# Kernel tuning notes

Measured on AMD Instinct MI355X. Metric: run time of the kernel, lower is better.

Reference implementation:

```python
import jax, jax.numpy as jnp
import numpy as np

B, S, E, H, HD, RD, MP = 2, 2048, 1024, 16, 64, 32, 8  # batch, seq, embed, heads, head_dim, rotary_dim, mp_num


def rotate_every_two(x):
    # x: [..., D] -> interleave (-x_odd, x_even)
    x1 = x[..., ::2]
    x2 = x[..., 1::2]
    return jnp.stack((-x2, x1), axis=-1).reshape(x.shape)


def apply_rotary(x, sin, cos):
    # x: [B,S,H,RD]; sin/cos: [S, RD//2] -> repeat_interleave(2) -> [1,S,1,RD]
    sin = jnp.repeat(sin, 2, axis=-1)[None, :, None, :]
    cos = jnp.repeat(cos, 2, axis=-1)[None, :, None, :]
    return x * cos + rotate_every_two(x) * sin


def setup_inputs() -> dict:
    key = jax.random.key(0)
    k1, k2, k3 = jax.random.split(key, 3)
    return {
        "hidden_states": jax.random.normal(k1, (B, S, E), dtype=jnp.float32),
        "w_qkv": jax.random.normal(k2, (3 * E, E), dtype=jnp.float32) * 0.02,
        "w_out": jax.random.normal(k3, (E, E), dtype=jnp.float32) * 0.02,
    }


def reference(hidden_states, w_qkv, w_out):
    qkv = hidden_states @ w_qkv.T                      # [B,S,3E]
    local = HD * H // MP                               # 128
    qkv = qkv.reshape(B, S, MP, 3 * local)
    # torch.split order in source is (query, value, key)
    q, v, k = jnp.split(qkv, 3, axis=-1)               # each [B,S,MP,local]

    def split_heads(x):
        return x.reshape(B, S, MP, H // MP, HD).reshape(B, S, H, HD)

    q, k, v = split_heads(q), split_heads(k), split_heads(v)  # [B,S,H,HD]

    # fixed sinusoidal rotary embedding over first RD dims
    inv_freq = 1.0 / 10000 ** (jnp.arange(0, RD, 2, dtype=jnp.float32) / RD)
    sinusoid = jnp.arange(S, dtype=jnp.float32)[:, None] * inv_freq[None, :]  # [S, RD//2]
    sin, cos = jnp.sin(sinusoid), jnp.cos(sinusoid)

    q = jnp.concatenate([apply_rotary(q[..., :RD], sin, cos), q[..., RD:]], axis=-1)
    k = jnp.concatenate([apply_rotary(k[..., :RD], sin, cos), k[..., RD:]], axis=-1)

    # [B,H,S,HD]
    q = q.transpose(0, 2, 1, 3)
    k = k.transpose(0, 2, 1, 3)
    v = v.transpose(0, 2, 1, 3)

    scores = jnp.einsum('bhqd,bhkd->bhqk', q, k) / np.float32(np.sqrt(HD))
    causal = jnp.tril(jnp.ones((S, S), dtype=bool))
    scores = jnp.where(causal[None, None], scores, jnp.float32(-1e9))
    attn = jax.nn.softmax(scores.astype(jnp.float32), axis=-1).astype(q.dtype)
    out = jnp.einsum('bhqk,bhkd->bhqd', attn, v)       # [B,H,S,HD]
    out = out.transpose(0, 2, 1, 3).reshape(B, S, E)
    return out @ w_out.T
```

## Files before the change

### kernel.cpp

```cpp
#include <hip/hip_runtime.h>

typedef __attribute__((ext_vector_type(8))) short short8;
typedef __attribute__((ext_vector_type(4))) float v4f;

#define ASYNC_COPY16(ldsptr, gptr)                                                        \
  __builtin_amdgcn_global_load_lds((const __attribute__((address_space(1))) void*)(gptr), \
                                   (__attribute__((address_space(3))) void*)(ldsptr),     \
                                   16, 0, 0)

__device__ __forceinline__ unsigned short f2bf(float f) {
  unsigned int u = __float_as_uint(f);
  u += 0x7fffu + ((u >> 16) & 1u);
  return (unsigned short)(u >> 16);
}
__device__ __forceinline__ float bf2f(unsigned short s) {
  return __uint_as_float(((unsigned int)s) << 16);
}

__global__ void convert_all(const float* __restrict__ h, const float* __restrict__ wq,
                            const float* __restrict__ wo, unsigned short* __restrict__ ho,
                            unsigned short* __restrict__ wqo, unsigned short* __restrict__ woo) {
  int i = (blockIdx.x * blockDim.x + threadIdx.x) * 4;
  const float* src;
  unsigned short* dst;
  int j;
  if (i < 4194304) { src = h; dst = ho; j = i; }
  else if (i < 7340032) { src = wq; dst = wqo; j = i - 4194304; }
  else { src = wo; dst = woo; j = i - 7340032; }
  float4 v = *(const float4*)(src + j);
  ushort4 o;
  o.x = f2bf(v.x); o.y = f2bf(v.y); o.z = f2bf(v.z); o.w = f2bf(v.w);
  *(ushort4*)(dst + j) = o;
}

template <int BN, bool BF16OUT>
__global__ __launch_bounds__(256) void gemm_bt(const unsigned short* __restrict__ A,
                                               const unsigned short* __restrict__ Bm,
                                               void* __restrict__ Cv, int M, int N, int K) {
  constexpr int WN = BN / 2;
  constexpr int JN = WN / 16;
  __shared__ __attribute__((aligned(16))) unsigned short As[128 * 32];
  __shared__ __attribute__((aligned(16))) unsigned short Bs[BN * 32];
  int t = threadIdx.x;
  int w = t >> 6, lane = t & 63, kb = lane >> 4, lr = lane & 15;
  int m0 = blockIdx.y * 128, n0 = blockIdx.x * BN;
  int wm = (w >> 1) * 64, wn = (w & 1) * WN;
  v4f acc[4][JN];
#pragma unroll
  for (int i = 0; i < 4; i++)
#pragma unroll
    for (int j = 0; j < JN; j++) acc[i][j] = (v4f){0.f, 0.f, 0.f, 0.f};
  int ra = m0 + (t >> 2);
  int rb = n0 + (t >> 2);
  int ca = (t & 3) * 8;
  for (int k0 = 0; k0 < K; k0 += 32) {
    ASYNC_COPY16(&As[t * 8],        A + (size_t)ra * K + k0 + ca);
    ASYNC_COPY16(&As[2048 + t * 8], A + (size_t)(ra + 64) * K + k0 + ca);
#pragma unroll
    for (int c = 0; c < BN / 64; c++)
      ASYNC_COPY16(&Bs[c * 2048 + t * 8], Bm + (size_t)(rb + c * 64) * K + k0 + ca);
    __syncthreads();
    short8 av[4], bv[JN];
#pragma unroll
    for (int i = 0; i < 4; i++) av[i] = *(const short8*)&As[(wm + i * 16 + lr) * 32 + kb * 8];
#pragma unroll
    for (int j = 0; j < JN; j++) bv[j] = *(const short8*)&Bs[(wn + j * 16 + lr) * 32 + kb * 8];
#pragma unroll
    for (int i = 0; i < 4; i++)
#pragma unroll
      for (int j = 0; j < JN; j++)
        acc[i][j] = __builtin_amdgcn_mfma_f32_16x16x32_bf16(av[i], bv[j], acc[i][j], 0, 0, 0);
    __syncthreads();
  }
#pragma unroll
  for (int i = 0; i < 4; i++) {
    int row = m0 + wm + i * 16 + kb * 4;
#pragma unroll
    for (int j = 0; j < JN; j++) {
      int col = n0 + wn + j * 16 + lr;
#pragma unroll
      for (int r = 0; r < 4; r++) {
        if (BF16OUT)
          ((unsigned short*)Cv)[(size_t)(row + r) * N + col] = f2bf(acc[i][j][r]);
        else
          ((float*)Cv)[(size_t)(row + r) * N + col] = acc[i][j][r];
      }
    }
  }
}

__global__ __launch_bounds__(256) void rope_vt(const unsigned short* __restrict__ qkv,
                                               unsigned short* __restrict__ Q,
                                               unsigned short* __restrict__ Ko,
                                               unsigned short* __restrict__ Vt) {
  __shared__ float tile[64][65];
  int t = threadIdx.x;
  int bh = blockIdx.y, s0 = blockIdx.x * 64;
  int b = bh >> 4, h = bh & 15;
  int mp = h >> 1, ii = h & 1;
  int hbase = mp * 384 + ii * 64;
  int tx = t & 63, ty = t >> 6;
#pragma unroll
  for (int q16 = 0; q16 < 16; q16++) {
    int srow = q16 * 4 + ty;
    tile[srow][tx] = bf2f(qkv[(size_t)(b * 2048 + s0 + srow) * 3072 + hbase + 128 + tx]);
  }
  int sl = t >> 2, ch = t & 3;
  int s = s0 + sl;
  size_t ib = (size_t)(b * 2048 + s) * 3072 + hbase + ch * 16;
  short8 qv0 = *(const short8*)(qkv + ib);
  short8 qv1 = *(const short8*)(qkv + ib + 8);
  short8 kv0 = *(const short8*)(qkv + ib + 256);
  short8 kv1 = *(const short8*)(qkv + ib + 264);
  float qf[16], kf[16];
#pragma unroll
  for (int j = 0; j < 8; j++) {
    qf[j] = bf2f((unsigned short)qv0[j]); qf[8 + j] = bf2f((unsigned short)qv1[j]);
    kf[j] = bf2f((unsigned short)kv0[j]); kf[8 + j] = bf2f((unsigned short)kv1[j]);
  }
  if (ch < 2) {
#pragma unroll
    for (int jj = 0; jj < 8; jj++) {
      int j = ch * 8 + jj;
      float ang = (float)s * expf(-(float)j * 0.57564627324851142f);
      float sn, cs;
      sincosf(ang, &sn, &cs);
      float a = qf[2 * jj], bq = qf[2 * jj + 1];
      qf[2 * jj] = a * cs - bq * sn; qf[2 * jj + 1] = bq * cs + a * sn;
      float c2 = kf[2 * jj], d2 = kf[2 * jj + 1];
      kf[2 * jj] = c2 * cs - d2 * sn; kf[2 * jj + 1] = d2 * cs + c2 * sn;
    }
  }
  const float qs = 0.125f * 1.4426950408889634f;
  unsigned short qo[16], ko[16];
#pragma unroll
  for (int j = 0; j < 16; j++) { qo[j] = f2bf(qs * qf[j]); ko[j] = f2bf(kf[j]); }
  size_t ob = (size_t)(bh * 2048 + s) * 64 + ch * 16;
  *(short8*)(Q + ob) = *(short8*)qo;
  *(short8*)(Q + ob + 8) = *(short8*)(qo + 8);
  *(short8*)(Ko + ob) = *(short8*)ko;
  *(short8*)(Ko + ob + 8) = *(short8*)(ko + 8);
  __syncthreads();
#pragma unroll
  for (int q16 = 0; q16 < 16; q16++) {
    int drow = q16 * 4 + ty;
    Vt[(size_t)bh * 64 * 2048 + (size_t)drow * 2048 + s0 + tx] = f2bf(tile[tx][drow]);
  }
}

__global__ __launch_bounds__(256) void attn_fused(const unsigned short* __restrict__ Qg,
                                                  const unsigned short* __restrict__ Kg,
                                                  const unsigned short* __restrict__ Vtg,
                                                  unsigned short* __restrict__ AO) {
  __shared__ __attribute__((aligned(16))) unsigned short Ks[2 * 128 * 64];
  __shared__ __attribute__((aligned(16))) unsigned short Vs[2 * 64 * 128];
  __shared__ __attribute__((aligned(16))) unsigned short Ps[4 * 32 * 64];
  int t = threadIdx.x;
  int w = t >> 6, lane = t & 63, kb = lane >> 4, lr = lane & 15;
  int wq = w >> 1, wk = w & 1;
  int gid = blockIdx.x;
  int bh = gid >> 4, pr = gid & 15;
  const unsigned short* Qb = Qg + (size_t)bh * 2048 * 64;
  const unsigned short* Kb = Kg + (size_t)bh * 2048 * 64;
  const unsigned short* Vb = Vtg + (size_t)bh * 64 * 2048;
  int b = bh >> 4, h = bh & 15;
  int sw = lr & 7;
  unsigned short* Pw = &Ps[w * 32 * 64];
  float* accS = (float*)Ps;
  float* lpS = (float*)Ks;

  auto stage = [&](int kt, int buf) {
    int base = buf * 8192;
#pragma unroll
    for (int rep = 0; rep < 4; rep++) {
      int s = rep * 256 + t;
      int krow = s >> 3;
      int kgc = (s & 7) ^ (krow & 7);
      ASYNC_COPY16(&Ks[base + s * 8], Kb + (size_t)(kt * 128 + krow) * 64 + kgc * 8);
      int vrow = s >> 4;
      int vgc = (s & 15) ^ (vrow & 7);
      ASYNC_COPY16(&Vs[base + s * 8], Vb + (size_t)vrow * 2048 + kt * 128 + vgc * 8);
    }
  };

  for (int half = 0; half < 2; half++) {
    int qtile = half ? (31 - pr) : pr;
    int m0 = qtile * 64;
    int nkt = (qtile >> 1) + 1;
    short8 aq[2][2];
#pragma unroll
    for (int m = 0; m < 2; m++) {
      int row = m0 + wq * 32 + m * 16 + lr;
#pragma unroll
      for (int c = 0; c < 2; c++)
        aq[m][c] = *(const short8*)(Qb + (size_t)row * 64 + c * 32 + kb * 8);
    }
    v4f acc[2][4];
    v4f lp[2];
#pragma unroll
    for (int m = 0; m < 2; m++) {
      lp[m] = (v4f){0.f, 0.f, 0.f, 0.f};
#pragma unroll
      for (int dt = 0; dt < 4; dt++) acc[m][dt] = (v4f){0.f, 0.f, 0.f, 0.f};
    }
    stage(0, 0);
    __syncthreads();
    for (int kt = 0; kt < nkt; kt++) {
      int cur = (kt & 1) * 8192;
      if (kt + 1 < nkt) stage(kt + 1, (kt + 1) & 1);
      v4f sc[2][4];
#pragma unroll
      for (int n = 0; n < 4; n++) {
        int krow = wk * 64 + n * 16 + lr;
        short8 bk0 = *(const short8*)&Ks[cur + krow * 64 + ((kb) ^ sw) * 8];
        short8 bk1 = *(const short8*)&Ks[cur + krow * 64 + ((kb + 4) ^ sw) * 8];
#pragma unroll
        for (int m = 0; m < 2; m++) {
          v4f z = (v4f){0.f, 0.f, 0.f, 0.f};
          z = __builtin_amdgcn_mfma_f32_16x16x32_bf16(aq[m][0], bk0, z, 0, 0, 0);
          z = __builtin_amdgcn_mfma_f32_16x16x32_bf16(aq[m][1], bk1, z, 0, 0, 0);
          sc[m][n] = z;
        }
      }
      if (kt == nkt - 1) {
#pragma unroll
        for (int m = 0; m < 2; m++)
#pragma unroll
          for (int n = 0; n < 4; n++)
#pragma unroll
            for (int r = 0; r < 4; r++) {
              int keya = kt * 128 + wk * 64 + n * 16 + lr;
              int qrow = m0 + wq * 32 + m * 16 + kb * 4 + r;
              if (keya > qrow) sc[m][n][r] = -1e30f;
            }
      }
#pragma unroll
      for (int m = 0; m < 2; m++)
#pragma unroll
        for (int n = 0; n < 4; n++)
#pragma unroll
          for (int r = 0; r < 4; r++) {
            float p = exp2f(sc[m][n][r]);
            lp[m][r] += p;
            int rp = m * 16 + kb * 4 + r;
            Pw[rp * 64 + ((n * 2 + (lr >> 3)) ^ (rp & 7)) * 8 + (lr & 7)] = f2bf(p);
          }
#pragma unroll
      for (int ks = 0; ks < 2; ks++) {
        short8 ap[2];
#pragma unroll
        for (int m = 0; m < 2; m++)
          ap[m] = *(const short8*)&Pw[(m * 16 + lr) * 64 + ((ks * 4 + kb) ^ sw) * 8];
#pragma unroll
        for (int dt = 0; dt < 4; dt++) {
          int d = dt * 16 + lr;
          short8 bv = *(const short8*)&Vs[cur + d * 128 + ((wk * 8 + ks * 4 + kb) ^ sw) * 8];
#pragma unroll
          for (int m = 0; m < 2; m++)
            acc[m][dt] = __builtin_amdgcn_mfma_f32_16x16x32_bf16(ap[m], bv, acc[m][dt], 0, 0, 0);
        }
      }
      __syncthreads();
    }
    if (wk == 1) {
#pragma unroll
      for (int m = 0; m < 2; m++) {
#pragma unroll
        for (int dt = 0; dt < 4; dt++)
          *(v4f*)&accS[wq * 2048 + (m * 4 + dt) * 256 + lane * 4] = acc[m][dt];
        *(v4f*)&lpS[wq * 512 + lane * 8 + m * 4] = lp[m];
      }
    }
    __syncthreads();
    if (wk == 0) {
#pragma unroll
      for (int m = 0; m < 2; m++) {
#pragma unroll
        for (int dt = 0; dt < 4; dt++)
          acc[m][dt] += *(v4f*)&accS[wq * 2048 + (m * 4 + dt) * 256 + lane * 4];
        lp[m] += *(v4f*)&lpS[wq * 512 + lane * 8 + m * 4];
      }
#pragma unroll
      for (int m = 0; m < 2; m++)
#pragma unroll
        for (int r = 0; r < 4; r++) {
          float s = lp[m][r];
#pragma unroll
          for (int off = 1; off < 16; off <<= 1) s += __shfl_xor(s, off);
          float inv = 1.0f / s;
          int qrow = m0 + wq * 32 + m * 16 + kb * 4 + r;
#pragma unroll
          for (int dt = 0; dt < 4; dt++)
            AO[(size_t)(b * 2048 + qrow) * 1024 + h * 64 + dt * 16 + lr] =
                f2bf(acc[m][dt][r] * inv);
        }
    }
    __syncthreads();
  }
}

extern "C" void kernel_launch(void* const* d_in, const int* in_sizes, int n_in,
                              void* d_out, int out_size, void* d_ws, size_t ws_size,
                              hipStream_t stream) {
  const float* hidden = (const float*)d_in[0];
  const float* w_qkv = (const float*)d_in[1];
  const float* w_out = (const float*)d_in[2];
  float* out = (float*)d_out;
  char* ws = (char*)d_ws;
  unsigned short* hid_bf = (unsigned short*)(ws);
  unsigned short* wqkv_bf = (unsigned short*)(ws + (8ull << 20));
  unsigned short* wout_bf = (unsigned short*)(ws + (14ull << 20));
  unsigned short* qkv_bf = (unsigned short*)(ws + (16ull << 20));
  unsigned short* Qb = (unsigned short*)(ws + (40ull << 20));
  unsigned short* Kb = (unsigned short*)(ws + (48ull << 20));
  unsigned short* Vt = (unsigned short*)(ws + (56ull << 20));
  unsigned short* AO = (unsigned short*)(ws + (64ull << 20));

  convert_all<<<8192, 256, 0, stream>>>(hidden, w_qkv, w_out, hid_bf, wqkv_bf, wout_bf);
  gemm_bt<128, true><<<dim3(24, 32), 256, 0, stream>>>(hid_bf, wqkv_bf, qkv_bf, 4096, 3072, 1024);
  rope_vt<<<dim3(32, 32), 256, 0, stream>>>(qkv_bf, Qb, Kb, Vt);
  attn_fused<<<512, 256, 0, stream>>>(Qb, Kb, Vt, AO);
  gemm_bt<64, false><<<dim3(16, 32), 256, 0, stream>>>(AO, wout_bf, out, 4096, 1024, 1024);
}
```

Before: 226.9 us.

## Restructure attention into one query tile per 128-thread block with 64-key tiles

The attention kernel no longer has each 256-thread block process a paired short and long query tile, with two wave pairs splitting the keys and merging partial results through LDS. It now launches 1024 blocks of 128 threads, each handling one 64-row query tile over 64-key tiles, with a rotated tile order to spread causal work. The per-block cross-wave reduction is gone. V is written in a permuted column order so each lane can store four packed bf16 P values at once, turning scalar LDS stores into 8-byte stores. The cost is less intra-block parallelism, more blocks with uneven causal work, and more loop iterations per key.

```diff
diff --git a/kernel.cpp b/kernel.cpp
--- a/kernel.cpp
+++ b/kernel.cpp
@@ -144,159 +144,142 @@
 #pragma unroll
   for (int q16 = 0; q16 < 16; q16++) {
     int drow = q16 * 4 + ty;
-    Vt[(size_t)bh * 64 * 2048 + (size_t)drow * 2048 + s0 + tx] = f2bf(tile[tx][drow]);
-  }
-}
-
-__global__ __launch_bounds__(256) void attn_fused(const unsigned short* __restrict__ Qg,
+    int p = (tx & 15) * 4 + (tx >> 4);
+    Vt[(size_t)bh * 64 * 2048 + (size_t)drow * 2048 + s0 + p] = f2bf(tile[tx][drow]);
+  }
+}
+
+__global__ __launch_bounds__(128) void attn_fused(const unsigned short* __restrict__ Qg,
                                                   const unsigned short* __restrict__ Kg,
                                                   const unsigned short* __restrict__ Vtg,
                                                   unsigned short* __restrict__ AO) {
-  __shared__ __attribute__((aligned(16))) unsigned short Ks[2 * 128 * 64];
-  __shared__ __attribute__((aligned(16))) unsigned short Vs[2 * 64 * 128];
-  __shared__ __attribute__((aligned(16))) unsigned short Ps[4 * 32 * 64];
+  __shared__ __attribute__((aligned(16))) unsigned short Ks[2 * 64 * 64];
+  __shared__ __attribute__((aligned(16))) unsigned short Vs[2 * 64 * 64];
+  __shared__ __attribute__((aligned(16))) unsigned short Ps[2 * 32 * 64];
   int t = threadIdx.x;
   int w = t >> 6, lane = t & 63, kb = lane >> 4, lr = lane & 15;
-  int wq = w >> 1, wk = w & 1;
   int gid = blockIdx.x;
-  int bh = gid >> 4, pr = gid & 15;
+  int bh = gid >> 5;
+  int qtile = ((gid & 31) + bh) & 31;
+  int m0 = qtile * 64;
   const unsigned short* Qb = Qg + (size_t)bh * 2048 * 64;
   const unsigned short* Kb = Kg + (size_t)bh * 2048 * 64;
   const unsigned short* Vb = Vtg + (size_t)bh * 64 * 2048;
-  int b = bh >> 4, h = bh & 15;
+
+  short8 aq[2][2];
+#pragma unroll
+  for (int m = 0; m < 2; m++) {
+    int row = m0 + w * 32 + m * 16 + lr;
+#pragma unroll
+    for (int c = 0; c < 2; c++)
+      aq[m][c] = *(const short8*)(Qb + (size_t)row * 64 + c * 32 + kb * 8);
+  }
+
+  v4f acc[2][4];
+  float lp[2][4];
+#pragma unroll
+  for (int m = 0; m < 2; m++) {
+#pragma unroll
+    for (int dt = 0; dt < 4; dt++) acc[m][dt] = (v4f){0.f, 0.f, 0.f, 0.f};
+#pragma unroll
+    for (int r = 0; r < 4; r++) lp[m][r] = 0.f;
+  }
+
+  int nkt = qtile + 1;
+
+  auto stage = [&](int kt, int buf) {
+    int base = buf * 4096;
+#pragma unroll
+    for (int rep = 0; rep < 4; rep++) {
+      int s = rep * 128 + t;
+      int row = s >> 3;
+      int gc = (s & 7) ^ (row & 7);
+      ASYNC_COPY16(&Ks[base + s * 8], Kb + (size_t)(kt * 64 + row) * 64 + gc * 8);
+      ASYNC_COPY16(&Vs[base + s * 8], Vb + (size_t)row * 2048 + kt * 64 + gc * 8);
+    }
+  };
+
+  stage(0, 0);
+  __syncthreads();
+
   int sw = lr & 7;
   unsigned short* Pw = &Ps[w * 32 * 64];
-  float* accS = (float*)Ps;
-  float* lpS = (float*)Ks;
-
-  auto stage = [&](int kt, int buf) {
-    int base = buf * 8192;
-#pragma unroll
-    for (int rep = 0; rep < 4; rep++) {
-      int s = rep * 256 + t;
-      int krow = s >> 3;
-      int kgc = (s & 7) ^ (krow & 7);
-      ASYNC_COPY16(&Ks[base + s * 8], Kb + (size_t)(kt * 128 + krow) * 64 + kgc * 8);
-      int vrow = s >> 4;
-      int vgc = (s & 15) ^ (vrow & 7);
-      ASYNC_COPY16(&Vs[base + s * 8], Vb + (size_t)vrow * 2048 + kt * 128 + vgc * 8);
-    }
-  };
-
-  for (int half = 0; half < 2; half++) {
-    int qtile = half ? (31 - pr) : pr;
-    int m0 = qtile * 64;
-    int nkt = (qtile >> 1) + 1;
-    short8 aq[2][2];
-#pragma unroll
-    for (int m = 0; m < 2; m++) {
-      int row = m0 + wq * 32 + m * 16 + lr;
-#pragma unroll
-      for (int c = 0; c < 2; c++)
-        aq[m][c] = *(const short8*)(Qb + (size_t)row * 64 + c * 32 + kb * 8);
-    }
-    v4f acc[2][4];
-    v4f lp[2];
-#pragma unroll
-    for (int m = 0; m < 2; m++) {
-      lp[m] = (v4f){0.f, 0.f, 0.f, 0.f};
-#pragma unroll
-      for (int dt = 0; dt < 4; dt++) acc[m][dt] = (v4f){0.f, 0.f, 0.f, 0.f};
-    }
-    stage(0, 0);
+  for (int kt = 0; kt < nkt; kt++) {
+    int cur = (kt & 1) * 4096;
+    if (kt + 1 < nkt) stage(kt + 1, (kt + 1) & 1);
+    v4f sc[2][4];
+#pragma unroll
+    for (int n2 = 0; n2 < 4; n2++) {
+      int krow = n2 * 16 + lr;
+      short8 bk0 = *(const short8*)&Ks[cur + krow * 64 + (kb ^ sw) * 8];
+      short8 bk1 = *(const short8*)&Ks[cur + krow * 64 + ((kb + 4) ^ sw) * 8];
+#pragma unroll
+      for (int m = 0; m < 2; m++) {
+        v4f z = (v4f){0.f, 0.f, 0.f, 0.f};
+        z = __builtin_amdgcn_mfma_f32_16x16x32_bf16(aq[m][0], bk0, z, 0, 0, 0);
+        z = __builtin_amdgcn_mfma_f32_16x16x32_bf16(aq[m][1], bk1, z, 0, 0, 0);
+        sc[m][n2] = z;
+      }
+    }
+    if (kt == nkt - 1) {
+#pragma unroll
+      for (int m = 0; m < 2; m++)
+#pragma unroll
+        for (int n2 = 0; n2 < 4; n2++)
+#pragma unroll
+          for (int r = 0; r < 4; r++) {
+            int key = kt * 64 + n2 * 16 + lr;
+            int qrow = m0 + w * 32 + m * 16 + kb * 4 + r;
+            if (key > qrow) sc[m][n2][r] = -1e30f;
+          }
+    }
+#pragma unroll
+    for (int m = 0; m < 2; m++)
+#pragma unroll
+      for (int r = 0; r < 4; r++) {
+        unsigned short pk[4];
+#pragma unroll
+        for (int n2 = 0; n2 < 4; n2++) {
+          float p = exp2f(sc[m][n2][r]);
+          lp[m][r] += p;
+          pk[n2] = f2bf(p);
+        }
+        int rp = m * 16 + kb * 4 + r;
+        int col = (((lr >> 1) ^ (rp & 7)) * 8) + (lr & 1) * 4;
+        *(uint2*)&Pw[rp * 64 + col] = *(uint2*)pk;
+      }
+#pragma unroll
+    for (int ks = 0; ks < 2; ks++) {
+      short8 ap[2];
+#pragma unroll
+      for (int m = 0; m < 2; m++)
+        ap[m] = *(const short8*)&Pw[(m * 16 + lr) * 64 + ((ks * 4 + kb) ^ sw) * 8];
+#pragma unroll
+      for (int dt = 0; dt < 4; dt++) {
+        int d = dt * 16 + lr;
+        short8 bv = *(const short8*)&Vs[cur + d * 64 + ((ks * 4 + kb) ^ sw) * 8];
+#pragma unroll
+        for (int m = 0; m < 2; m++)
+          acc[m][dt] = __builtin_amdgcn_mfma_f32_16x16x32_bf16(ap[m], bv, acc[m][dt], 0, 0, 0);
+      }
+    }
     __syncthreads();
-    for (int kt = 0; kt < nkt; kt++) {
-      int cur = (kt & 1) * 8192;
-      if (kt + 1 < nkt) stage(kt + 1, (kt + 1) & 1);
-      v4f sc[2][4];
-#pragma unroll
-      for (int n = 0; n < 4; n++) {
-        int krow = wk * 64 + n * 16 + lr;
-        short8 bk0 = *(const short8*)&Ks[cur + krow * 64 + ((kb) ^ sw) * 8];
-        short8 bk1 = *(const short8*)&Ks[cur + krow * 64 + ((kb + 4) ^ sw) * 8];
-#pragma unroll
-        for (int m = 0; m < 2; m++) {
-          v4f z = (v4f){0.f, 0.f, 0.f, 0.f};
-          z = __builtin_amdgcn_mfma_f32_16x16x32_bf16(aq[m][0], bk0, z, 0, 0, 0);
-          z = __builtin_amdgcn_mfma_f32_16x16x32_bf16(aq[m][1], bk1, z, 0, 0, 0);
-          sc[m][n] = z;
-        }
-      }
-      if (kt == nkt - 1) {
-#pragma unroll
-        for (int m = 0; m < 2; m++)
-#pragma unroll
-          for (int n = 0; n < 4; n++)
-#pragma unroll
-            for (int r = 0; r < 4; r++) {
-              int keya = kt * 128 + wk * 64 + n * 16 + lr;
-              int qrow = m0 + wq * 32 + m * 16 + kb * 4 + r;
-              if (keya > qrow) sc[m][n][r] = -1e30f;
-            }
-      }
-#pragma unroll
-      for (int m = 0; m < 2; m++)
-#pragma unroll
-        for (int n = 0; n < 4; n++)
-#pragma unroll
-          for (int r = 0; r < 4; r++) {
-            float p = exp2f(sc[m][n][r]);
-            lp[m][r] += p;
-            int rp = m * 16 + kb * 4 + r;
-            Pw[rp * 64 + ((n * 2 + (lr >> 3)) ^ (rp & 7)) * 8 + (lr & 7)] = f2bf(p);
-          }
-#pragma unroll
-      for (int ks = 0; ks < 2; ks++) {
-        short8 ap[2];
-#pragma unroll
-        for (int m = 0; m < 2; m++)
-          ap[m] = *(const short8*)&Pw[(m * 16 + lr) * 64 + ((ks * 4 + kb) ^ sw) * 8];
-#pragma unroll
-        for (int dt = 0; dt < 4; dt++) {
-          int d = dt * 16 + lr;
-          short8 bv = *(const short8*)&Vs[cur + d * 128 + ((wk * 8 + ks * 4 + kb) ^ sw) * 8];
-#pragma unroll
-          for (int m = 0; m < 2; m++)
-            acc[m][dt] = __builtin_amdgcn_mfma_f32_16x16x32_bf16(ap[m], bv, acc[m][dt], 0, 0, 0);
-        }
-      }
-      __syncthreads();
-    }
-    if (wk == 1) {
-#pragma unroll
-      for (int m = 0; m < 2; m++) {
-#pragma unroll
-        for (int dt = 0; dt < 4; dt++)
-          *(v4f*)&accS[wq * 2048 + (m * 4 + dt) * 256 + lane * 4] = acc[m][dt];
-        *(v4f*)&lpS[wq * 512 + lane * 8 + m * 4] = lp[m];
-      }
-    }
-    __syncthreads();
-    if (wk == 0) {
-#pragma unroll
-      for (int m = 0; m < 2; m++) {
-#pragma unroll
-        for (int dt = 0; dt < 4; dt++)
-          acc[m][dt] += *(v4f*)&accS[wq * 2048 + (m * 4 + dt) * 256 + lane * 4];
-        lp[m] += *(v4f*)&lpS[wq * 512 + lane * 8 + m * 4];
-      }
-#pragma unroll
-      for (int m = 0; m < 2; m++)
-#pragma unroll
-        for (int r = 0; r < 4; r++) {
-          float s = lp[m][r];
-#pragma unroll
-          for (int off = 1; off < 16; off <<= 1) s += __shfl_xor(s, off);
-          float inv = 1.0f / s;
-          int qrow = m0 + wq * 32 + m * 16 + kb * 4 + r;
-#pragma unroll
-          for (int dt = 0; dt < 4; dt++)
-            AO[(size_t)(b * 2048 + qrow) * 1024 + h * 64 + dt * 16 + lr] =
-                f2bf(acc[m][dt][r] * inv);
-        }
-    }
-    __syncthreads();
-  }
+  }
+  int b = bh >> 4, h = bh & 15;
+#pragma unroll
+  for (int m = 0; m < 2; m++)
+#pragma unroll
+    for (int r = 0; r < 4; r++) {
+      float s = lp[m][r];
+#pragma unroll
+      for (int off = 1; off < 16; off <<= 1) s += __shfl_xor(s, off);
+      float inv = 1.0f / s;
+      int qrow = m0 + w * 32 + m * 16 + kb * 4 + r;
+#pragma unroll
+      for (int dt = 0; dt < 4; dt++)
+        AO[(size_t)(b * 2048 + qrow) * 1024 + h * 64 + dt * 16 + lr] =
+            f2bf(acc[m][dt][r] * inv);
+    }
 }
 
 extern "C" void kernel_launch(void* const* d_in, const int* in_sizes, int n_in,
@@ -319,6 +302,6 @@
   convert_all<<<8192, 256, 0, stream>>>(hidden, w_qkv, w_out, hid_bf, wqkv_bf, wout_bf);
   gemm_bt<128, true><<<dim3(24, 32), 256, 0, stream>>>(hid_bf, wqkv_bf, qkv_bf, 4096, 3072, 1024);
   rope_vt<<<dim3(32, 32), 256, 0, stream>>>(qkv_bf, Qb, Kb, Vt);
-  attn_fused<<<512, 256, 0, stream>>>(Qb, Kb, Vt, AO);
+  attn_fused<<<1024, 128, 0, stream>>>(Qb, Kb, Vt, AO);
   gemm_bt<64, false><<<dim3(16, 32), 256, 0, stream>>>(AO, wout_bf, out, 4096, 1024, 1024);
 }
```

After: 253.6 us. 11.8% more time.
